# Kernel tuning notes

Hardware: AMD Instinct MI355X
Metric: run time of the kernel (lower is better)

Reference implementation:

```python
import jax, jax.numpy as jnp
import numpy as np

NUM_EVENT, EVENT_DIM = 6, 32
NUM_WORD, WORD_DIM = 100000, 128
NUM_SKU, SKU_DIM = 500000, 128
NUM_CAT, CAT_DIM = 10000, 64
NUM_PRICE, PRICE_DIM = 100, 32
NUM_URL, URL_DIM = 200000, 128
HIDDEN = 512
B, S, W = 256, 256, 12
PAD = 0


def _table(key, n, d):
    t = jax.random.normal(key, (n, d), dtype=jnp.float32) * 0.02
    return t.at[PAD].set(0.0)  # padding_idx row is zero


def setup_inputs() -> dict:
    key = jax.random.key(0)
    ks = jax.random.split(key, 20)
    inp = {
        "event_table": _table(ks[0], NUM_EVENT, EVENT_DIM),
        "word_table": _table(ks[1], NUM_WORD, WORD_DIM),
        "sku_table": _table(ks[2], NUM_SKU, SKU_DIM),
        "cat_table": _table(ks[3], NUM_CAT, CAT_DIM),
        "price_table": _table(ks[4], NUM_PRICE, PRICE_DIM),
        "url_table": _table(ks[5], NUM_URL, URL_DIM),
        # Linear weights, torch convention: y = x @ W.T + b
        "sku_w": jax.random.normal(ks[6], (HIDDEN, EVENT_DIM + SKU_DIM + CAT_DIM + PRICE_DIM + WORD_DIM), dtype=jnp.float32) * 0.02,
        "sku_b": jnp.zeros((HIDDEN,), dtype=jnp.float32),
        "url_w": jax.random.normal(ks[7], (HIDDEN, URL_DIM + EVENT_DIM), dtype=jnp.float32) * 0.02,
        "url_b": jnp.zeros((HIDDEN,), dtype=jnp.float32),
        "query_w": jax.random.normal(ks[8], (HIDDEN, EVENT_DIM + WORD_DIM), dtype=jnp.float32) * 0.02,
        "query_b": jnp.zeros((HIDDEN,), dtype=jnp.float32),
        "event_type": jax.random.randint(ks[9], (B, S), 0, NUM_EVENT, dtype=jnp.int32),
        "sku_id": jax.random.randint(ks[10], (B, S), 0, NUM_SKU, dtype=jnp.int32),
        "url_id": jax.random.randint(ks[11], (B, S), 0, NUM_URL, dtype=jnp.int32),
        "cat_id": jax.random.randint(ks[12], (B, S), 0, NUM_CAT, dtype=jnp.int32),
        "price_id": jax.random.randint(ks[13], (B, S), 0, NUM_PRICE, dtype=jnp.int32),
        "word_id": jax.random.randint(ks[14], (B, S, W), 0, NUM_WORD, dtype=jnp.int32),
    }
    return inp


def _linear_relu(x, w, b):
    return jax.nn.relu(jnp.einsum("bsi,hi->bsh", x, w) + b)


def reference(event_table, word_table, sku_table, cat_table, price_table, url_table,
              sku_w, sku_b, url_w, url_b, query_w, query_b,
              event_type, sku_id, url_id, cat_id, price_id, word_id):
    # padding mask: 1.0 where event_type == PAD_IDX
    src_padding_mask = (event_type == PAD).astype(jnp.float32)

    event_emb = event_table[event_type]                 # [B,S,E]
    word_emb = word_table[word_id].mean(axis=-2)        # [B,S,Wd] (WordEmbedding avg)

    # SKU branch (event types 1,2,3): concat(event, sku, cat, price, word)
    sku_in = jnp.concatenate([event_emb, sku_table[sku_id], cat_table[cat_id],
                              price_table[price_id], word_emb], axis=-1)
    sku_out = _linear_relu(sku_in, sku_w, sku_b)        # [B,S,H]

    # URL branch (event type 4): concat(url, event)  -- note order in UrlEmbedding
    url_in = jnp.concatenate([url_table[url_id], event_emb], axis=-1)
    url_out = _linear_relu(url_in, url_w, url_b)

    # Query branch (event type 5): concat(event, word)
    query_in = jnp.concatenate([event_emb, word_emb], axis=-1)
    query_out = _linear_relu(query_in, query_w, query_b)

    is_sku = ((event_type >= 1) & (event_type <= 3))[..., None]
    is_url = (event_type == 4)[..., None]
    is_query = (event_type == 5)[..., None]

    seq_emb = (jnp.where(is_sku, sku_out, 0.0)
               + jnp.where(is_url, url_out, 0.0)
               + jnp.where(is_query, query_out, 0.0))   # PAD positions stay zero
    return seq_emb, src_padding_mask
```

## Files before the change

### kernel.cpp

```cpp
#include <hip/hip_runtime.h>
#include <hip/hip_bf16.h>
#if !__has_builtin(__builtin_amdgcn_cvt_pk_fp8_f32) || !__has_builtin(__builtin_amdgcn_cvt_pk_f32_fp8)
#include <hip/hip_fp8.h>
#endif

#define CUR_OFF   0
#define SLOT_OFF  1024
#define POS_OFF   263168
#define WSKU_OFF  1049600
#define WURL_OFF  1246208
#define WQRY_OFF  1344512
#define WF8_OFF   2097152
#define XS_OFF    16777216
#define XU_OFF    50331648
#define XQ_OFF    68157440

#define NPOS      65536
#define OUT_MASK  33554432
#define F8_SCALE  64.0f
#define INV4096   (1.0f / 4096.0f)

typedef __attribute__((ext_vector_type(4))) float f32x4;
typedef __attribute__((ext_vector_type(2))) float f32x2;
typedef __attribute__((ext_vector_type(2))) unsigned int u32x2;

__device__ __forceinline__ float2 ld2(const float* p) {
    return *reinterpret_cast<const float2*>(p);
}

__device__ __forceinline__ unsigned int pk2_f8(float a, float b) {
#if __has_builtin(__builtin_amdgcn_cvt_pk_fp8_f32)
    return __builtin_amdgcn_cvt_pk_fp8_f32(a, b, 0u, false);
#else
    __hip_fp8_e4m3 fa(a), fb(b);
    return (unsigned int)fa.__x | ((unsigned int)fb.__x << 8);
#endif
}
__device__ __forceinline__ unsigned int pk4_f8(float a, float b, float c, float d) {
#if __has_builtin(__builtin_amdgcn_cvt_pk_fp8_f32)
    unsigned int v = 0;
    v = __builtin_amdgcn_cvt_pk_fp8_f32(a, b, v, false);
    v = __builtin_amdgcn_cvt_pk_fp8_f32(c, d, v, true);
    return v;
#else
    return pk2_f8(a, b) | (pk2_f8(c, d) << 16);
#endif
}
__device__ __forceinline__ float2 upk2_f8(unsigned int u) {
#if __has_builtin(__builtin_amdgcn_cvt_pk_f32_fp8)
    f32x2 r = __builtin_amdgcn_cvt_pk_f32_fp8(u, false);
    return make_float2(r.x, r.y);
#else
    __hip_fp8_e4m3 fa, fb;
    fa.__x = (unsigned char)(u & 0xff);
    fb.__x = (unsigned char)((u >> 8) & 0xff);
    return make_float2((float)fa, (float)fb);
#endif
}
__device__ __forceinline__ void st_f8x2(unsigned char* d, float a, float b) {
    *reinterpret_cast<unsigned short*>(d) = (unsigned short)(pk2_f8(a, b) & 0xffffu);
}

#define AS1(p) ((const __attribute__((address_space(1))) void*)(p))
#define AS3(p) ((__attribute__((address_space(3))) void*)(p))

__global__ __launch_bounds__(256) void prep_k(const float* __restrict__ sw,
                                              const float* __restrict__ uw,
                                              const float* __restrict__ qw,
                                              const float* __restrict__ word_t,
                                              char* ws) {
    const int b = blockIdx.x, t = threadIdx.x;
    if (b < 6250) {
        size_t i = ((size_t)b * 256 + t) * 8;
        f32x4 v0 = *reinterpret_cast<const f32x4*>(word_t + i);
        f32x4 v1 = *reinterpret_cast<const f32x4*>(word_t + i + 4);
        u32x2 pk;
        pk.x = pk4_f8(v0.x * F8_SCALE, v0.y * F8_SCALE, v0.z * F8_SCALE, v0.w * F8_SCALE);
        pk.y = pk4_f8(v1.x * F8_SCALE, v1.y * F8_SCALE, v1.z * F8_SCALE, v1.w * F8_SCALE);
        *reinterpret_cast<u32x2*>((unsigned char*)(ws + WF8_OFF) + i) = pk;
        return;
    }
    int tt = (b - 6250) * 256 + t;
    if (tt < 3) ((int*)(ws + CUR_OFF))[tt] = 0;
    if (tt < 196608) {
        ((unsigned char*)(ws + WSKU_OFF))[tt] =
            (unsigned char)(pk2_f8(sw[tt] * F8_SCALE, 0.f) & 0xffu);
    } else if (tt < 294912) {
        int i = tt - 196608; int n = i / 192, k = i % 192;
        ((unsigned char*)(ws + WURL_OFF))[i] = (k < 160)
            ? (unsigned char)(pk2_f8(uw[n * 160 + k] * F8_SCALE, 0.f) & 0xffu) : 0;
    } else {
        int i = tt - 294912; int n = i / 192, k = i % 192;
        ((unsigned char*)(ws + WQRY_OFF))[i] = (k < 160)
            ? (unsigned char)(pk2_f8(qw[n * 160 + k] * F8_SCALE, 0.f) & 0xffu) : 0;
    }
}

__global__ __launch_bounds__(256) void alloc_k(const int* __restrict__ et_a,
                                               float* __restrict__ out, char* ws) {
    __shared__ int s_wcnt[4][3];
    __shared__ int s_base[3];
    __shared__ int s_woff[4][3];
    const int t = threadIdx.x, lane = t & 63, wid = t >> 6;
    int p = blockIdx.x * 256 + t;
    int et = et_a[p];
    int br = (et >= 1 && et <= 3) ? 0 : (et == 4 ? 1 : (et == 5 ? 2 : -1));
    unsigned long long m0 = __ballot(br == 0);
    unsigned long long m1 = __ballot(br == 1);
    unsigned long long m2 = __ballot(br == 2);
    if (lane == 0) {
        s_wcnt[wid][0] = (int)__popcll(m0);
        s_wcnt[wid][1] = (int)__popcll(m1);
        s_wcnt[wid][2] = (int)__popcll(m2);
    }
    __syncthreads();
    if (t < 3) {
        int c0 = s_wcnt[0][t], c1 = s_wcnt[1][t], c2 = s_wcnt[2][t], c3 = s_wcnt[3][t];
        int tot = c0 + c1 + c2 + c3;
        s_base[t] = tot ? atomicAdd(&((int*)(ws + CUR_OFF))[t], tot) : 0;
        s_woff[0][t] = 0; s_woff[1][t] = c0; s_woff[2][t] = c0 + c1; s_woff[3][t] = c0 + c1 + c2;
    }
    __syncthreads();
    unsigned long long lt = (1ull << lane) - 1ull;
    int slot = -1;
    if (br == 0)      slot = s_base[0] + s_woff[wid][0] + (int)__popcll(m0 & lt);
    else if (br == 1) slot = s_base[1] + s_woff[wid][1] + (int)__popcll(m1 & lt);
    else if (br == 2) slot = s_base[2] + s_woff[wid][2] + (int)__popcll(m2 & lt);
    ((int*)(ws + SLOT_OFF))[p] = slot;
    if (slot >= 0) ((int*)(ws + POS_OFF))[br * NPOS + slot] = p;
    __builtin_nontemporal_store((et == 0) ? 1.0f : 0.0f, &out[OUT_MASK + p]);
}

__device__ __forceinline__ float2 wsum_f8(const unsigned char* __restrict__ wt8,
                                          const int* __restrict__ wids, int lane) {
    float sx = 0.f, sy = 0.f;
    #pragma unroll
    for (int k = 0; k < 12; ++k) {
        unsigned int u = *reinterpret_cast<const unsigned short*>(
            wt8 + (size_t)wids[k] * 128 + 2 * lane);
        float2 v = upk2_f8(u);
        sx += v.x; sy += v.y;
    }
    const float inv = 1.0f / 12.0f;
    return make_float2(sx * inv, sy * inv);
}

__global__ __launch_bounds__(256) void build_k(
    const float* __restrict__ ev_t,
    const float* __restrict__ sku_t,  const float* __restrict__ cat_t,
    const float* __restrict__ price_t,const float* __restrict__ url_t,
    const int* __restrict__ et_a,     const int* __restrict__ sku_id,
    const int* __restrict__ url_id,   const int* __restrict__ cat_id,
    const int* __restrict__ price_id, const int* __restrict__ word_id,
    float* __restrict__ out, char* ws)
{
    const int t = threadIdx.x, lane = t & 63, wid = t >> 6;
    const int p = blockIdx.x * 4 + wid;
    const int et = et_a[p];
    if (et == 0) {
        f32x4 z = {0.f, 0.f, 0.f, 0.f};
        float* orow = out + (size_t)p * 512;
        __builtin_nontemporal_store(z, reinterpret_cast<f32x4*>(&orow[lane * 8]));
        __builtin_nontemporal_store(z, reinterpret_cast<f32x4*>(&orow[lane * 8 + 4]));
        return;
    }
    const int slot = ((const int*)(ws + SLOT_OFF))[p];
    const unsigned char* wf8 = (const unsigned char*)(ws + WF8_OFF);
    const float* evr = ev_t + et * 32;
    if (et <= 3) {
        unsigned char* X = (unsigned char*)(ws + XS_OFF) + (size_t)slot * 384;
        if (lane < 16) { float2 e = ld2(evr + 2 * lane);
                         st_f8x2(X + 2 * lane, e.x * F8_SCALE, e.y * F8_SCALE); }
        const float* sr = sku_t + (size_t)sku_id[p] * 128;
        { float2 s = ld2(sr + 2 * lane);
          st_f8x2(X + 32 + 2 * lane, s.x * F8_SCALE, s.y * F8_SCALE); }
        if (lane < 32) { const float* cr = cat_t + (size_t)cat_id[p] * 64;
                         float2 c = ld2(cr + 2 * lane);
                         st_f8x2(X + 160 + 2 * lane, c.x * F8_SCALE, c.y * F8_SCALE); }
        if (lane < 16) { const float* pr = price_t + (size_t)price_id[p] * 32;
                         float2 v = ld2(pr + 2 * lane);
                         st_f8x2(X + 224 + 2 * lane, v.x * F8_SCALE, v.y * F8_SCALE); }
        float2 w = wsum_f8(wf8, word_id + (size_t)p * 12, lane);
        st_f8x2(X + 256 + 2 * lane, w.x, w.y);
    } else if (et == 4) {
        unsigned char* X = (unsigned char*)(ws + XU_OFF) + (size_t)slot * 192;
        const float* ur = url_t + (size_t)url_id[p] * 128;
        { float2 u = ld2(ur + 2 * lane);
          st_f8x2(X + 2 * lane, u.x * F8_SCALE, u.y * F8_SCALE); }
        if (lane < 16) { float2 e = ld2(evr + 2 * lane);
                         st_f8x2(X + 128 + 2 * lane, e.x * F8_SCALE, e.y * F8_SCALE); }
        if (lane >= 48) *reinterpret_cast<unsigned short*>(X + 160 + 2 * (lane - 48)) = 0;
    } else {
        unsigned char* X = (unsigned char*)(ws + XQ_OFF) + (size_t)slot * 192;
        if (lane < 16) { float2 e = ld2(evr + 2 * lane);
                         st_f8x2(X + 2 * lane, e.x * F8_SCALE, e.y * F8_SCALE); }
        float2 w = wsum_f8(wf8, word_id + (size_t)p * 12, lane);
        st_f8x2(X + 32 + 2 * lane, w.x, w.y);
        if (lane >= 48) *reinterpret_cast<unsigned short*>(X + 160 + 2 * (lane - 48)) = 0;
    }
}

__global__ __launch_bounds__(256, 2) void gemm_all_k(
    const char* __restrict__ ws_c, const float* __restrict__ sku_b,
    const float* __restrict__ url_b, const float* __restrict__ qry_b,
    float* __restrict__ out)
{
    const int z = blockIdx.z;
    const int count = ((const int*)(ws_c + CUR_OFF))[z];
    const int nmt = (count + 127) >> 7;
    const int nwg = nmt * 4;
    const int orig = blockIdx.x;
    if (orig >= nwg) return;
    const int q8 = nwg >> 3, r8 = nwg & 7;
    const int xcd = orig & 7, idx = orig >> 3;
    const int wg = (xcd < r8 ? xcd * (q8 + 1) : r8 * (q8 + 1) + (xcd - r8) * q8) + idx;
    const int mt = wg >> 2;
    const int row0 = mt * 128;
    const int nc0  = (wg & 3) * 128;

    const char* arena; const char* Wb; const float* bias; const int* posm;
    int astride, nkt;
    if (z == 0) { arena = ws_c + XS_OFF; Wb = ws_c + WSKU_OFF; bias = sku_b;
                  posm = (const int*)(ws_c + POS_OFF);          astride = 384; nkt = 3; }
    else if (z == 1) { arena = ws_c + XU_OFF; Wb = ws_c + WURL_OFF; bias = url_b;
                  posm = (const int*)(ws_c + POS_OFF) + NPOS;   astride = 192; nkt = 2; }
    else       { arena = ws_c + XQ_OFF; Wb = ws_c + WQRY_OFF; bias = qry_b;
                  posm = (const int*)(ws_c + POS_OFF) + 2*NPOS; astride = 192; nkt = 2; }

    __shared__ char lds[2][2][16384];

    const int t = threadIdx.x;
    const int lane = t & 63;
    const int wid  = t >> 6;
    const int wr = wid >> 1, wc = wid & 1;
    const int r = lane & 15, q = lane >> 4;

    auto stage = [&](int buf, int koff, bool full) {
        if (full) {
            #pragma unroll
            for (int i = 0; i < 4; ++i) {
                int row = i * 32 + (t >> 3);
                int sb  = (t & 7) ^ (row & 7);
                const char* ga = arena + (size_t)(row0 + row) * astride + koff + sb * 16;
                __builtin_amdgcn_global_load_lds(AS1(ga), AS3(&lds[buf][0][i * 4096 + t * 16]), 16, 0, 0);
                const char* gb = Wb + (size_t)(nc0 + row) * astride + koff + sb * 16;
                __builtin_amdgcn_global_load_lds(AS1(gb), AS3(&lds[buf][1][i * 4096 + t * 16]), 16, 0, 0);
            }
        } else {
            #pragma unroll
            for (int i = 0; i < 2; ++i) {
                int row = i * 64 + (t >> 2);
                int sb  = (t & 3) ^ (row & 3);
                const char* ga = arena + (size_t)(row0 + row) * astride + koff + sb * 16;
                __builtin_amdgcn_global_load_lds(AS1(ga), AS3(&lds[buf][0][i * 4096 + t * 16]), 16, 0, 0);
                const char* gb = Wb + (size_t)(nc0 + row) * astride + koff + sb * 16;
                __builtin_amdgcn_global_load_lds(AS1(gb), AS3(&lds[buf][1][i * 4096 + t * 16]), 16, 0, 0);
            }
        }
    };

    f32x4 acc[4][4];
    #pragma unroll
    for (int m = 0; m < 4; ++m)
        #pragma unroll
        for (int n = 0; n < 4; ++n)
            acc[m][n] = (f32x4){0.f, 0.f, 0.f, 0.f};

    stage(0, 0, true);
    __syncthreads();
    int cur = 0;
    for (int kt = 0; kt < nkt; ++kt) {
        const bool full = (z == 0) || (kt == 0);
        if (kt + 1 < nkt) stage(cur ^ 1, (kt + 1) * 128, (z == 0));
        if (full) {
            #pragma unroll
            for (int kk = 0; kk < 4; ++kk) {
                const int u  = kk * 2 + (q >> 1);
                const int wo = (q & 1) * 8;
                long af[4], bfr[4];
                #pragma unroll
                for (int m = 0; m < 4; ++m) {
                    int arow = wr * 64 + m * 16 + r;
                    af[m] = *reinterpret_cast<const long*>(
                        &lds[cur][0][arow * 128 + ((u ^ (arow & 7)) << 4) + wo]);
                }
                #pragma unroll
                for (int n = 0; n < 4; ++n) {
                    int brow = wc * 64 + n * 16 + r;
                    bfr[n] = *reinterpret_cast<const long*>(
                        &lds[cur][1][brow * 128 + ((u ^ (brow & 7)) << 4) + wo]);
                }
                #pragma unroll
                for (int m = 0; m < 4; ++m)
                    #pragma unroll
                    for (int n = 0; n < 4; ++n)
                        acc[m][n] = __builtin_amdgcn_mfma_f32_16x16x32_fp8_fp8(af[m], bfr[n], acc[m][n], 0, 0, 0);
            }
        } else {
            #pragma unroll
            for (int kk = 0; kk < 2; ++kk) {
                const int u  = kk * 2 + (q >> 1);
                const int wo = (q & 1) * 8;
                long af[4], bfr[4];
                #pragma unroll
                for (int m = 0; m < 4; ++m) {
                    int arow = wr * 64 + m * 16 + r;
                    af[m] = *reinterpret_cast<const long*>(
                        &lds[cur][0][arow * 64 + ((u ^ (arow & 3)) << 4) + wo]);
                }
                #pragma unroll
                for (int n = 0; n < 4; ++n) {
                    int brow = wc * 64 + n * 16 + r;
                    bfr[n] = *reinterpret_cast<const long*>(
                        &lds[cur][1][brow * 64 + ((u ^ (brow & 3)) << 4) + wo]);
                }
                #pragma unroll
                for (int m = 0; m < 4; ++m)
                    #pragma unroll
                    for (int n = 0; n < 4; ++n)
                        acc[m][n] = __builtin_amdgcn_mfma_f32_16x16x32_fp8_fp8(af[m], bfr[n], acc[m][n], 0, 0, 0);
            }
        }
        __syncthreads();
        cur ^= 1;
    }

    float bv[4];
    #pragma unroll
    for (int n = 0; n < 4; ++n) bv[n] = bias[nc0 + wc * 64 + n * 16 + r];
    #pragma unroll
    for (int m = 0; m < 4; ++m) {
        #pragma unroll
        for (int j = 0; j < 4; ++j) {
            int rl = wr * 64 + m * 16 + q * 4 + j;
            int gr = row0 + rl;
            if (gr < count) {
                int pos = posm[gr];
                float* orow = out + (size_t)pos * 512 + nc0 + wc * 64;
                #pragma unroll
                for (int n = 0; n < 4; ++n)
                    __builtin_nontemporal_store(
                        fmaxf(acc[m][n][j] * INV4096 + bv[n], 0.f), &orow[n * 16 + r]);
            }
        }
    }
}

extern "C" void kernel_launch(void* const* d_in, const int* in_sizes, int n_in,
                              void* d_out, int out_size, void* d_ws, size_t ws_size,
                              hipStream_t stream) {
    const float* ev_t    = (const float*)d_in[0];
    const float* word_t  = (const float*)d_in[1];
    const float* sku_t   = (const float*)d_in[2];
    const float* cat_t   = (const float*)d_in[3];
    const float* price_t = (const float*)d_in[4];
    const float* url_t   = (const float*)d_in[5];
    const float* sku_w   = (const float*)d_in[6];
    const float* sku_b   = (const float*)d_in[7];
    const float* url_w   = (const float*)d_in[8];
    const float* url_b   = (const float*)d_in[9];
    const float* query_w = (const float*)d_in[10];
    const float* query_b = (const float*)d_in[11];
    const int* event_type = (const int*)d_in[12];
    const int* sku_id     = (const int*)d_in[13];
    const int* url_id     = (const int*)d_in[14];
    const int* cat_id     = (const int*)d_in[15];
    const int* price_id   = (const int*)d_in[16];
    const int* word_id    = (const int*)d_in[17];

    char*  ws  = (char*)d_ws;
    float* out = (float*)d_out;

    prep_k<<<7786, 256, 0, stream>>>(sku_w, url_w, query_w, word_t, ws);
    alloc_k<<<256, 256, 0, stream>>>(event_type, out, ws);
    build_k<<<16384, 256, 0, stream>>>(ev_t, sku_t, cat_t, price_t, url_t,
                                       event_type, sku_id, url_id, cat_id, price_id,
                                       word_id, out, ws);
    dim3 gg(2048, 1, 3);
    gemm_all_k<<<gg, 256, 0, stream>>>(ws, sku_b, url_b, query_b, out);
}
```

Baseline: 86.76 us.

## Unroll GEMM K-loop with explicit vmcnt waits and raw barriers

Replaces the generic double-buffered K loop with fully unrolled per-branch schedules that issue two stages up front and use partial s_waitcnt vmcnt counts plus raw s_barrier instead of __syncthreads. This lets the second tile's async global-to-LDS loads stay in flight while the first tile is computed, removing full memory drains at each step. It relies on hand-counted outstanding load numbers and sched_barrier fences, so any miscount or compiler-inserted memory op could cause races.

After: 86.21 us (median of 2 runs). Within noise of the previous version (-0.6%).

```diff
diff --git a/kernel.cpp b/kernel.cpp
--- a/kernel.cpp
+++ b/kernel.cpp
@@ -63,6 +63,13 @@
 
 #define AS1(p) ((const __attribute__((address_space(1))) void*)(p))
 #define AS3(p) ((__attribute__((address_space(3))) void*)(p))
+
+#define WAITV0() asm volatile("s_waitcnt vmcnt(0)" ::: "memory")
+#define WAITV4() asm volatile("s_waitcnt vmcnt(4)" ::: "memory")
+#define WAITV8() asm volatile("s_waitcnt vmcnt(8)" ::: "memory")
+#define WAITL()  asm volatile("s_waitcnt lgkmcnt(0)" ::: "memory")
+#define BARR()   __builtin_amdgcn_s_barrier()
+#define FENCE()  __builtin_amdgcn_sched_barrier(0)
 
 __global__ __launch_bounds__(256) void prep_k(const float* __restrict__ sw,
                                               const float* __restrict__ uw,
@@ -219,13 +226,13 @@
     const int nc0  = (wg & 3) * 128;
 
     const char* arena; const char* Wb; const float* bias; const int* posm;
-    int astride, nkt;
+    int astride;
     if (z == 0) { arena = ws_c + XS_OFF; Wb = ws_c + WSKU_OFF; bias = sku_b;
-                  posm = (const int*)(ws_c + POS_OFF);          astride = 384; nkt = 3; }
+                  posm = (const int*)(ws_c + POS_OFF);          astride = 384; }
     else if (z == 1) { arena = ws_c + XU_OFF; Wb = ws_c + WURL_OFF; bias = url_b;
-                  posm = (const int*)(ws_c + POS_OFF) + NPOS;   astride = 192; nkt = 2; }
+                  posm = (const int*)(ws_c + POS_OFF) + NPOS;   astride = 192; }
     else       { arena = ws_c + XQ_OFF; Wb = ws_c + WQRY_OFF; bias = qry_b;
-                  posm = (const int*)(ws_c + POS_OFF) + 2*NPOS; astride = 192; nkt = 2; }
+                  posm = (const int*)(ws_c + POS_OFF) + 2*NPOS; astride = 192; }
 
     __shared__ char lds[2][2][16384];
 
@@ -235,27 +242,26 @@
     const int wr = wid >> 1, wc = wid & 1;
     const int r = lane & 15, q = lane >> 4;
 
-    auto stage = [&](int buf, int koff, bool full) {
-        if (full) {
-            #pragma unroll
-            for (int i = 0; i < 4; ++i) {
-                int row = i * 32 + (t >> 3);
-                int sb  = (t & 7) ^ (row & 7);
-                const char* ga = arena + (size_t)(row0 + row) * astride + koff + sb * 16;
-                __builtin_amdgcn_global_load_lds(AS1(ga), AS3(&lds[buf][0][i * 4096 + t * 16]), 16, 0, 0);
-                const char* gb = Wb + (size_t)(nc0 + row) * astride + koff + sb * 16;
-                __builtin_amdgcn_global_load_lds(AS1(gb), AS3(&lds[buf][1][i * 4096 + t * 16]), 16, 0, 0);
-            }
-        } else {
-            #pragma unroll
-            for (int i = 0; i < 2; ++i) {
-                int row = i * 64 + (t >> 2);
-                int sb  = (t & 3) ^ (row & 3);
-                const char* ga = arena + (size_t)(row0 + row) * astride + koff + sb * 16;
-                __builtin_amdgcn_global_load_lds(AS1(ga), AS3(&lds[buf][0][i * 4096 + t * 16]), 16, 0, 0);
-                const char* gb = Wb + (size_t)(nc0 + row) * astride + koff + sb * 16;
-                __builtin_amdgcn_global_load_lds(AS1(gb), AS3(&lds[buf][1][i * 4096 + t * 16]), 16, 0, 0);
-            }
+    auto stage_full = [&](int buf, int koff) {
+        #pragma unroll
+        for (int i = 0; i < 4; ++i) {
+            int row = i * 32 + (t >> 3);
+            int sb  = (t & 7) ^ (row & 7);
+            const char* ga = arena + (size_t)(row0 + row) * astride + koff + sb * 16;
+            __builtin_amdgcn_global_load_lds(AS1(ga), AS3(&lds[buf][0][i * 4096 + t * 16]), 16, 0, 0);
+            const char* gb = Wb + (size_t)(nc0 + row) * astride + koff + sb * 16;
+            __builtin_amdgcn_global_load_lds(AS1(gb), AS3(&lds[buf][1][i * 4096 + t * 16]), 16, 0, 0);
+        }
+    };
+    auto stage_half = [&](int buf, int koff) {
+        #pragma unroll
+        for (int i = 0; i < 2; ++i) {
+            int row = i * 64 + (t >> 2);
+            int sb  = (t & 3) ^ (row & 3);
+            const char* ga = arena + (size_t)(row0 + row) * astride + koff + sb * 16;
+            __builtin_amdgcn_global_load_lds(AS1(ga), AS3(&lds[buf][0][i * 4096 + t * 16]), 16, 0, 0);
+            const char* gb = Wb + (size_t)(nc0 + row) * astride + koff + sb * 16;
+            __builtin_amdgcn_global_load_lds(AS1(gb), AS3(&lds[buf][1][i * 4096 + t * 16]), 16, 0, 0);
         }
     };
 
@@ -266,63 +272,75 @@
         for (int n = 0; n < 4; ++n)
             acc[m][n] = (f32x4){0.f, 0.f, 0.f, 0.f};
 
-    stage(0, 0, true);
-    __syncthreads();
-    int cur = 0;
-    for (int kt = 0; kt < nkt; ++kt) {
-        const bool full = (z == 0) || (kt == 0);
-        if (kt + 1 < nkt) stage(cur ^ 1, (kt + 1) * 128, (z == 0));
-        if (full) {
-            #pragma unroll
-            for (int kk = 0; kk < 4; ++kk) {
-                const int u  = kk * 2 + (q >> 1);
-                const int wo = (q & 1) * 8;
-                long af[4], bfr[4];
+    auto comp_full = [&](int buf) {
+        #pragma unroll
+        for (int kk = 0; kk < 4; ++kk) {
+            const int u  = kk * 2 + (q >> 1);
+            const int wo = (q & 1) * 8;
+            long af[4], bfr[4];
+            #pragma unroll
+            for (int m = 0; m < 4; ++m) {
+                int arow = wr * 64 + m * 16 + r;
+                af[m] = *reinterpret_cast<const long*>(
+                    &lds[buf][0][arow * 128 + ((u ^ (arow & 7)) << 4) + wo]);
+            }
+            #pragma unroll
+            for (int n = 0; n < 4; ++n) {
+                int brow = wc * 64 + n * 16 + r;
+                bfr[n] = *reinterpret_cast<const long*>(
+                    &lds[buf][1][brow * 128 + ((u ^ (brow & 7)) << 4) + wo]);
+            }
+            #pragma unroll
+            for (int m = 0; m < 4; ++m)
                 #pragma unroll
-                for (int m = 0; m < 4; ++m) {
-                    int arow = wr * 64 + m * 16 + r;
-                    af[m] = *reinterpret_cast<const long*>(
-                        &lds[cur][0][arow * 128 + ((u ^ (arow & 7)) << 4) + wo]);
-                }
+                for (int n = 0; n < 4; ++n)
+                    acc[m][n] = __builtin_amdgcn_mfma_f32_16x16x32_fp8_fp8(af[m], bfr[n], acc[m][n], 0, 0, 0);
+        }
+    };
+    auto comp_half = [&](int buf) {
+        #pragma unroll
+        for (int kk = 0; kk < 2; ++kk) {
+            const int u  = kk * 2 + (q >> 1);
+            const int wo = (q & 1) * 8;
+            long af[4], bfr[4];
+            #pragma unroll
+            for (int m = 0; m < 4; ++m) {
+                int arow = wr * 64 + m * 16 + r;
+                af[m] = *reinterpret_cast<const long*>(
+                    &lds[buf][0][arow * 64 + ((u ^ (arow & 3)) << 4) + wo]);
+            }
+            #pragma unroll
+            for (int n = 0; n < 4; ++n) {
+                int brow = wc * 64 + n * 16 + r;
+                bfr[n] = *reinterpret_cast<const long*>(
+                    &lds[buf][1][brow * 64 + ((u ^ (brow & 3)) << 4) + wo]);
+            }
+            #pragma unroll
+            for (int m = 0; m < 4; ++m)
                 #pragma unroll
-                for (int n = 0; n < 4; ++n) {
-                    int brow = wc * 64 + n * 16 + r;
-                    bfr[n] = *reinterpret_cast<const long*>(
-                        &lds[cur][1][brow * 128 + ((u ^ (brow & 7)) << 4) + wo]);
-                }
-                #pragma unroll
-                for (int m = 0; m < 4; ++m)
-                    #pragma unroll
-                    for (int n = 0; n < 4; ++n)
-                        acc[m][n] = __builtin_amdgcn_mfma_f32_16x16x32_fp8_fp8(af[m], bfr[n], acc[m][n], 0, 0, 0);
-            }
-        } else {
-            #pragma unroll
-            for (int kk = 0; kk < 2; ++kk) {
-                const int u  = kk * 2 + (q >> 1);
-                const int wo = (q & 1) * 8;
-                long af[4], bfr[4];
-                #pragma unroll
-                for (int m = 0; m < 4; ++m) {
-                    int arow = wr * 64 + m * 16 + r;
-                    af[m] = *reinterpret_cast<const long*>(
-                        &lds[cur][0][arow * 64 + ((u ^ (arow & 3)) << 4) + wo]);
-                }
-                #pragma unroll
-                for (int n = 0; n < 4; ++n) {
-                    int brow = wc * 64 + n * 16 + r;
-                    bfr[n] = *reinterpret_cast<const long*>(
-                        &lds[cur][1][brow * 64 + ((u ^ (brow & 3)) << 4) + wo]);
-                }
-                #pragma unroll
-                for (int m = 0; m < 4; ++m)
-                    #pragma unroll
-                    for (int n = 0; n < 4; ++n)
-                        acc[m][n] = __builtin_amdgcn_mfma_f32_16x16x32_fp8_fp8(af[m], bfr[n], acc[m][n], 0, 0, 0);
-            }
-        }
-        __syncthreads();
-        cur ^= 1;
+                for (int n = 0; n < 4; ++n)
+                    acc[m][n] = __builtin_amdgcn_mfma_f32_16x16x32_fp8_fp8(af[m], bfr[n], acc[m][n], 0, 0, 0);
+        }
+    };
+
+    if (z == 0) {
+        stage_full(0, 0);
+        stage_full(1, 128);
+        WAITV8(); BARR(); FENCE();
+        comp_full(0);
+        WAITL(); BARR(); FENCE();
+        stage_full(0, 256);
+        WAITV8(); BARR(); FENCE();
+        comp_full(1);
+        WAITV0(); BARR(); FENCE();
+        comp_full(0);
+    } else {
+        stage_full(0, 0);
+        stage_half(1, 128);
+        WAITV4(); BARR(); FENCE();
+        comp_full(0);
+        WAITV0(); BARR(); FENCE();
+        comp_half(1);
     }
 
     float bv[4];
```

## Fuse embedding gather into GEMM, keeping A tile resident across all N chunks

Applied to the files above, without the earlier changes.

The separate build kernel that gathered embeddings into fp8 staging arenas in global memory is removed. The GEMM kernel now gathers each 128-row A tile directly into LDS once and loops over all four 128-column N chunks, streaming only the weight tiles with double buffering. Zeroing of padding rows moves into the allocation kernel. This removes the global round trip for the activation matrix and one kernel launch, but the gather is now serialized inside the GEMM blocks, and the grid shrinks fourfold with more LDS per block.

New measurement: 137.0 us. +57.9%, slower.

```diff
diff --git a/kernel.cpp b/kernel.cpp
--- a/kernel.cpp
+++ b/kernel.cpp
@@ -11,9 +11,6 @@
 #define WURL_OFF  1246208
 #define WQRY_OFF  1344512
 #define WF8_OFF   2097152
-#define XS_OFF    16777216
-#define XU_OFF    50331648
-#define XQ_OFF    68157440
 
 #define NPOS      65536
 #define OUT_MASK  33554432
@@ -56,9 +53,6 @@
     fb.__x = (unsigned char)((u >> 8) & 0xff);
     return make_float2((float)fa, (float)fb);
 #endif
-}
-__device__ __forceinline__ void st_f8x2(unsigned char* d, float a, float b) {
-    *reinterpret_cast<unsigned short*>(d) = (unsigned short)(pk2_f8(a, b) & 0xffffu);
 }
 
 #define AS1(p) ((const __attribute__((address_space(1))) void*)(p))
@@ -101,9 +95,12 @@
     __shared__ int s_wcnt[4][3];
     __shared__ int s_base[3];
     __shared__ int s_woff[4][3];
+    __shared__ int s_et[256];
     const int t = threadIdx.x, lane = t & 63, wid = t >> 6;
-    int p = blockIdx.x * 256 + t;
+    const int p0 = blockIdx.x * 256;
+    int p = p0 + t;
     int et = et_a[p];
+    s_et[t] = et;
     int br = (et >= 1 && et <= 3) ? 0 : (et == 4 ? 1 : (et == 5 ? 2 : -1));
     unsigned long long m0 = __ballot(br == 0);
     unsigned long long m1 = __ballot(br == 1);
@@ -129,6 +126,14 @@
     ((int*)(ws + SLOT_OFF))[p] = slot;
     if (slot >= 0) ((int*)(ws + POS_OFF))[br * NPOS + slot] = p;
     __builtin_nontemporal_store((et == 0) ? 1.0f : 0.0f, &out[OUT_MASK + p]);
+    for (int i = wid; i < 256; i += 4) {
+        if (s_et[i] == 0) {
+            float* orow = out + (size_t)(p0 + i) * 512;
+            f32x4 z = {0.f, 0.f, 0.f, 0.f};
+            __builtin_nontemporal_store(z, reinterpret_cast<f32x4*>(&orow[lane * 8]));
+            __builtin_nontemporal_store(z, reinterpret_cast<f32x4*>(&orow[lane * 8 + 4]));
+        }
+    }
 }
 
 __device__ __forceinline__ float2 wsum_f8(const unsigned char* __restrict__ wt8,
@@ -145,203 +150,227 @@
     return make_float2(sx * inv, sy * inv);
 }
 
-__global__ __launch_bounds__(256) void build_k(
-    const float* __restrict__ ev_t,
-    const float* __restrict__ sku_t,  const float* __restrict__ cat_t,
-    const float* __restrict__ price_t,const float* __restrict__ url_t,
+__global__ __launch_bounds__(256, 2) void ggemm_k(
+    const char* __restrict__ ws_c,
+    const float* __restrict__ ev_t,   const float* __restrict__ sku_t,
+    const float* __restrict__ cat_t,  const float* __restrict__ price_t,
+    const float* __restrict__ url_t,
     const int* __restrict__ et_a,     const int* __restrict__ sku_id,
     const int* __restrict__ url_id,   const int* __restrict__ cat_id,
     const int* __restrict__ price_id, const int* __restrict__ word_id,
-    float* __restrict__ out, char* ws)
-{
-    const int t = threadIdx.x, lane = t & 63, wid = t >> 6;
-    const int p = blockIdx.x * 4 + wid;
-    const int et = et_a[p];
-    if (et == 0) {
-        f32x4 z = {0.f, 0.f, 0.f, 0.f};
-        float* orow = out + (size_t)p * 512;
-        __builtin_nontemporal_store(z, reinterpret_cast<f32x4*>(&orow[lane * 8]));
-        __builtin_nontemporal_store(z, reinterpret_cast<f32x4*>(&orow[lane * 8 + 4]));
-        return;
-    }
-    const int slot = ((const int*)(ws + SLOT_OFF))[p];
-    const unsigned char* wf8 = (const unsigned char*)(ws + WF8_OFF);
-    const float* evr = ev_t + et * 32;
-    if (et <= 3) {
-        unsigned char* X = (unsigned char*)(ws + XS_OFF) + (size_t)slot * 384;
-        if (lane < 16) { float2 e = ld2(evr + 2 * lane);
-                         st_f8x2(X + 2 * lane, e.x * F8_SCALE, e.y * F8_SCALE); }
-        const float* sr = sku_t + (size_t)sku_id[p] * 128;
-        { float2 s = ld2(sr + 2 * lane);
-          st_f8x2(X + 32 + 2 * lane, s.x * F8_SCALE, s.y * F8_SCALE); }
-        if (lane < 32) { const float* cr = cat_t + (size_t)cat_id[p] * 64;
-                         float2 c = ld2(cr + 2 * lane);
-                         st_f8x2(X + 160 + 2 * lane, c.x * F8_SCALE, c.y * F8_SCALE); }
-        if (lane < 16) { const float* pr = price_t + (size_t)price_id[p] * 32;
-                         float2 v = ld2(pr + 2 * lane);
-                         st_f8x2(X + 224 + 2 * lane, v.x * F8_SCALE, v.y * F8_SCALE); }
-        float2 w = wsum_f8(wf8, word_id + (size_t)p * 12, lane);
-        st_f8x2(X + 256 + 2 * lane, w.x, w.y);
-    } else if (et == 4) {
-        unsigned char* X = (unsigned char*)(ws + XU_OFF) + (size_t)slot * 192;
-        const float* ur = url_t + (size_t)url_id[p] * 128;
-        { float2 u = ld2(ur + 2 * lane);
-          st_f8x2(X + 2 * lane, u.x * F8_SCALE, u.y * F8_SCALE); }
-        if (lane < 16) { float2 e = ld2(evr + 2 * lane);
-                         st_f8x2(X + 128 + 2 * lane, e.x * F8_SCALE, e.y * F8_SCALE); }
-        if (lane >= 48) *reinterpret_cast<unsigned short*>(X + 160 + 2 * (lane - 48)) = 0;
-    } else {
-        unsigned char* X = (unsigned char*)(ws + XQ_OFF) + (size_t)slot * 192;
-        if (lane < 16) { float2 e = ld2(evr + 2 * lane);
-                         st_f8x2(X + 2 * lane, e.x * F8_SCALE, e.y * F8_SCALE); }
-        float2 w = wsum_f8(wf8, word_id + (size_t)p * 12, lane);
-        st_f8x2(X + 32 + 2 * lane, w.x, w.y);
-        if (lane >= 48) *reinterpret_cast<unsigned short*>(X + 160 + 2 * (lane - 48)) = 0;
-    }
-}
-
-__global__ __launch_bounds__(256, 2) void gemm_all_k(
-    const char* __restrict__ ws_c, const float* __restrict__ sku_b,
-    const float* __restrict__ url_b, const float* __restrict__ qry_b,
-    float* __restrict__ out)
+    const float* __restrict__ sku_b,  const float* __restrict__ url_b,
+    const float* __restrict__ qry_b,  float* __restrict__ out)
 {
     const int z = blockIdx.z;
     const int count = ((const int*)(ws_c + CUR_OFF))[z];
     const int nmt = (count + 127) >> 7;
-    const int nwg = nmt * 4;
     const int orig = blockIdx.x;
-    if (orig >= nwg) return;
-    const int q8 = nwg >> 3, r8 = nwg & 7;
+    if (orig >= nmt) return;
+    const int q8 = nmt >> 3, r8 = nmt & 7;
     const int xcd = orig & 7, idx = orig >> 3;
-    const int wg = (xcd < r8 ? xcd * (q8 + 1) : r8 * (q8 + 1) + (xcd - r8) * q8) + idx;
-    const int mt = wg >> 2;
+    const int mt = (xcd < r8 ? xcd * (q8 + 1) : r8 * (q8 + 1) + (xcd - r8) * q8) + idx;
     const int row0 = mt * 128;
-    const int nc0  = (wg & 3) * 128;
-
-    const char* arena; const char* Wb; const float* bias; const int* posm;
-    int astride, nkt;
-    if (z == 0) { arena = ws_c + XS_OFF; Wb = ws_c + WSKU_OFF; bias = sku_b;
-                  posm = (const int*)(ws_c + POS_OFF);          astride = 384; nkt = 3; }
-    else if (z == 1) { arena = ws_c + XU_OFF; Wb = ws_c + WURL_OFF; bias = url_b;
-                  posm = (const int*)(ws_c + POS_OFF) + NPOS;   astride = 192; nkt = 2; }
-    else       { arena = ws_c + XQ_OFF; Wb = ws_c + WQRY_OFF; bias = qry_b;
-                  posm = (const int*)(ws_c + POS_OFF) + 2*NPOS; astride = 192; nkt = 2; }
-
-    __shared__ char lds[2][2][16384];
-
-    const int t = threadIdx.x;
-    const int lane = t & 63;
-    const int wid  = t >> 6;
+
+    const int* posm = (const int*)(ws_c + POS_OFF) + z * NPOS;
+    const unsigned char* wf8 = (const unsigned char*)(ws_c + WF8_OFF);
+    const char* Wb; const float* bias; int wstride;
+    if (z == 0)      { Wb = ws_c + WSKU_OFF; bias = sku_b; wstride = 384; }
+    else if (z == 1) { Wb = ws_c + WURL_OFF; bias = url_b; wstride = 192; }
+    else             { Wb = ws_c + WQRY_OFF; bias = qry_b; wstride = 192; }
+
+    __shared__ char ldsA[49152];
+    __shared__ char ldsB[2][16384];
+
+    const int t = threadIdx.x, lane = t & 63, wid = t >> 6;
     const int wr = wid >> 1, wc = wid & 1;
     const int r = lane & 15, q = lane >> 4;
 
-    auto stage = [&](int buf, int koff, bool full) {
-        if (full) {
-            #pragma unroll
-            for (int i = 0; i < 4; ++i) {
-                int row = i * 32 + (t >> 3);
-                int sb  = (t & 7) ^ (row & 7);
-                const char* ga = arena + (size_t)(row0 + row) * astride + koff + sb * 16;
-                __builtin_amdgcn_global_load_lds(AS1(ga), AS3(&lds[buf][0][i * 4096 + t * 16]), 16, 0, 0);
-                const char* gb = Wb + (size_t)(nc0 + row) * astride + koff + sb * 16;
-                __builtin_amdgcn_global_load_lds(AS1(gb), AS3(&lds[buf][1][i * 4096 + t * 16]), 16, 0, 0);
-            }
+    auto stA384 = [&](int row, int off, unsigned int pk) {
+        int kt = off >> 7, o = off & 127, u = o >> 4;
+        int addr = kt * 16384 + row * 128 + (((u ^ (row & 7)) << 4) | (o & 15));
+        *reinterpret_cast<unsigned short*>(ldsA + addr) = (unsigned short)(pk & 0xffffu);
+    };
+    auto stA192 = [&](int row, int off, unsigned int pk) {
+        int addr;
+        if (off < 128) { int u = off >> 4;
+            addr = row * 128 + (((u ^ (row & 7)) << 4) | (off & 15)); }
+        else { int o = off - 128; int u = o >> 4;
+            addr = 16384 + row * 64 + (((u ^ (row & 3)) << 4) | (o & 15)); }
+        *reinterpret_cast<unsigned short*>(ldsA + addr) = (unsigned short)(pk & 0xffffu);
+    };
+
+    auto stageB_full = [&](int buf, int nc, int koff) {
+        #pragma unroll
+        for (int i = 0; i < 4; ++i) {
+            int row = i * 32 + (t >> 3);
+            int sb  = (t & 7) ^ (row & 7);
+            const char* gb = Wb + (size_t)(nc * 128 + row) * wstride + koff + sb * 16;
+            __builtin_amdgcn_global_load_lds(AS1(gb), AS3(&ldsB[buf][i * 4096 + t * 16]), 16, 0, 0);
+        }
+    };
+    auto stageB_half = [&](int buf, int nc, int koff) {
+        #pragma unroll
+        for (int i = 0; i < 2; ++i) {
+            int row = i * 64 + (t >> 2);
+            int sb  = (t & 3) ^ (row & 3);
+            const char* gb = Wb + (size_t)(nc * 128 + row) * wstride + koff + sb * 16;
+            __builtin_amdgcn_global_load_lds(AS1(gb), AS3(&ldsB[buf][i * 4096 + t * 16]), 16, 0, 0);
+        }
+    };
+
+    stageB_full(0, 0, 0);
+    if (z == 0) stageB_full(1, 0, 128); else stageB_half(1, 0, 128);
+
+    for (int i = 0; i < 32; ++i) {
+        int row = (wid << 5) + i;
+        int gr  = row0 + row;
+        if (gr >= count) break;
+        int p = posm[gr];
+        if (z == 0) {
+            int et = et_a[p];
+            const float* evr = ev_t + et * 32;
+            if (lane < 16) { float2 e = ld2(evr + 2 * lane);
+                stA384(row, 2 * lane, pk2_f8(e.x * F8_SCALE, e.y * F8_SCALE)); }
+            { float2 s = ld2(sku_t + (size_t)sku_id[p] * 128 + 2 * lane);
+                stA384(row, 32 + 2 * lane, pk2_f8(s.x * F8_SCALE, s.y * F8_SCALE)); }
+            if (lane < 32) { float2 c = ld2(cat_t + (size_t)cat_id[p] * 64 + 2 * lane);
+                stA384(row, 160 + 2 * lane, pk2_f8(c.x * F8_SCALE, c.y * F8_SCALE)); }
+            if (lane < 16) { float2 v = ld2(price_t + (size_t)price_id[p] * 32 + 2 * lane);
+                stA384(row, 224 + 2 * lane, pk2_f8(v.x * F8_SCALE, v.y * F8_SCALE)); }
+            float2 w = wsum_f8(wf8, word_id + (size_t)p * 12, lane);
+            stA384(row, 256 + 2 * lane, pk2_f8(w.x, w.y));
+        } else if (z == 1) {
+            const float* evr = ev_t + 4 * 32;
+            { float2 u = ld2(url_t + (size_t)url_id[p] * 128 + 2 * lane);
+                stA192(row, 2 * lane, pk2_f8(u.x * F8_SCALE, u.y * F8_SCALE)); }
+            if (lane < 16) { float2 e = ld2(evr + 2 * lane);
+                stA192(row, 128 + 2 * lane, pk2_f8(e.x * F8_SCALE, e.y * F8_SCALE)); }
+            if (lane >= 48) stA192(row, 160 + 2 * (lane - 48), 0u);
         } else {
-            #pragma unroll
-            for (int i = 0; i < 2; ++i) {
-                int row = i * 64 + (t >> 2);
-                int sb  = (t & 3) ^ (row & 3);
-                const char* ga = arena + (size_t)(row0 + row) * astride + koff + sb * 16;
-                __builtin_amdgcn_global_load_lds(AS1(ga), AS3(&lds[buf][0][i * 4096 + t * 16]), 16, 0, 0);
-                const char* gb = Wb + (size_t)(nc0 + row) * astride + koff + sb * 16;
-                __builtin_amdgcn_global_load_lds(AS1(gb), AS3(&lds[buf][1][i * 4096 + t * 16]), 16, 0, 0);
-            }
-        }
-    };
-
-    f32x4 acc[4][4];
+            const float* evr = ev_t + 5 * 32;
+            if (lane < 16) { float2 e = ld2(evr + 2 * lane);
+                stA192(row, 2 * lane, pk2_f8(e.x * F8_SCALE, e.y * F8_SCALE)); }
+            float2 w = wsum_f8(wf8, word_id + (size_t)p * 12, lane);
+            stA192(row, 32 + 2 * lane, pk2_f8(w.x, w.y));
+            if (lane >= 48) stA192(row, 160 + 2 * (lane - 48), 0u);
+        }
+    }
+    __syncthreads();
+
+    int posr[16];
     #pragma unroll
     for (int m = 0; m < 4; ++m)
         #pragma unroll
-        for (int n = 0; n < 4; ++n)
-            acc[m][n] = (f32x4){0.f, 0.f, 0.f, 0.f};
-
-    stage(0, 0, true);
-    __syncthreads();
-    int cur = 0;
-    for (int kt = 0; kt < nkt; ++kt) {
-        const bool full = (z == 0) || (kt == 0);
-        if (kt + 1 < nkt) stage(cur ^ 1, (kt + 1) * 128, (z == 0));
-        if (full) {
-            #pragma unroll
-            for (int kk = 0; kk < 4; ++kk) {
-                const int u  = kk * 2 + (q >> 1);
-                const int wo = (q & 1) * 8;
-                long af[4], bfr[4];
+        for (int j = 0; j < 4; ++j) {
+            int gr = row0 + wr * 64 + m * 16 + q * 4 + j;
+            posr[m * 4 + j] = (gr < count) ? posm[gr] : -1;
+        }
+
+    f32x4 acc[4][4];
+    auto compA_full = [&](int ktA, int buf) {
+        #pragma unroll
+        for (int kk = 0; kk < 4; ++kk) {
+            const int u  = kk * 2 + (q >> 1);
+            const int wo = (q & 1) * 8;
+            long af[4], bf[4];
+            #pragma unroll
+            for (int m = 0; m < 4; ++m) {
+                int arow = wr * 64 + m * 16 + r;
+                af[m] = *reinterpret_cast<const long*>(
+                    &ldsA[ktA * 16384 + arow * 128 + ((u ^ (arow & 7)) << 4) + wo]);
+            }
+            #pragma unroll
+            for (int n = 0; n < 4; ++n) {
+                int brow = wc * 64 + n * 16 + r;
+                bf[n] = *reinterpret_cast<const long*>(
+                    &ldsB[buf][brow * 128 + ((u ^ (brow & 7)) << 4) + wo]);
+            }
+            #pragma unroll
+            for (int m = 0; m < 4; ++m)
                 #pragma unroll
-                for (int m = 0; m < 4; ++m) {
-                    int arow = wr * 64 + m * 16 + r;
-                    af[m] = *reinterpret_cast<const long*>(
-                        &lds[cur][0][arow * 128 + ((u ^ (arow & 7)) << 4) + wo]);
-                }
+                for (int n = 0; n < 4; ++n)
+                    acc[m][n] = __builtin_amdgcn_mfma_f32_16x16x32_fp8_fp8(af[m], bf[n], acc[m][n], 0, 0, 0);
+        }
+    };
+    auto compA_half = [&](int buf) {
+        #pragma unroll
+        for (int kk = 0; kk < 2; ++kk) {
+            const int u  = kk * 2 + (q >> 1);
+            const int wo = (q & 1) * 8;
+            long af[4], bf[4];
+            #pragma unroll
+            for (int m = 0; m < 4; ++m) {
+                int arow = wr * 64 + m * 16 + r;
+                af[m] = *reinterpret_cast<const long*>(
+                    &ldsA[16384 + arow * 64 + ((u ^ (arow & 3)) << 4) + wo]);
+            }
+            #pragma unroll
+            for (int n = 0; n < 4; ++n) {
+                int brow = wc * 64 + n * 16 + r;
+                bf[n] = *reinterpret_cast<const long*>(
+                    &ldsB[buf][brow * 64 + ((u ^ (brow & 3)) << 4) + wo]);
+            }
+            #pragma unroll
+            for (int m = 0; m < 4; ++m)
                 #pragma unroll
-                for (int n = 0; n < 4; ++n) {
-                    int brow = wc * 64 + n * 16 + r;
-                    bfr[n] = *reinterpret_cast<const long*>(
-                        &lds[cur][1][brow * 128 + ((u ^ (brow & 7)) << 4) + wo]);
-                }
-                #pragma unroll
-                for (int m = 0; m < 4; ++m)
+                for (int n = 0; n < 4; ++n)
+                    acc[m][n] = __builtin_amdgcn_mfma_f32_16x16x32_fp8_fp8(af[m], bf[n], acc[m][n], 0, 0, 0);
+        }
+    };
+    auto epilogue = [&](int nc) {
+        float bv[4];
+        #pragma unroll
+        for (int n = 0; n < 4; ++n) bv[n] = bias[nc * 128 + wc * 64 + n * 16 + r];
+        #pragma unroll
+        for (int m = 0; m < 4; ++m)
+            #pragma unroll
+            for (int j = 0; j < 4; ++j) {
+                int pos = posr[m * 4 + j];
+                if (pos >= 0) {
+                    float* orow = out + (size_t)pos * 512 + nc * 128 + wc * 64;
                     #pragma unroll
                     for (int n = 0; n < 4; ++n)
-                        acc[m][n] = __builtin_amdgcn_mfma_f32_16x16x32_fp8_fp8(af[m], bfr[n], acc[m][n], 0, 0, 0);
-            }
-        } else {
-            #pragma unroll
-            for (int kk = 0; kk < 2; ++kk) {
-                const int u  = kk * 2 + (q >> 1);
-                const int wo = (q & 1) * 8;
-                long af[4], bfr[4];
-                #pragma unroll
-                for (int m = 0; m < 4; ++m) {
-                    int arow = wr * 64 + m * 16 + r;
-                    af[m] = *reinterpret_cast<const long*>(
-                        &lds[cur][0][arow * 64 + ((u ^ (arow & 3)) << 4) + wo]);
+                        __builtin_nontemporal_store(
+                            fmaxf(acc[m][n][j] * INV4096 + bv[n], 0.f), &orow[n * 16 + r]);
                 }
-                #pragma unroll
-                for (int n = 0; n < 4; ++n) {
-                    int brow = wc * 64 + n * 16 + r;
-                    bfr[n] = *reinterpret_cast<const long*>(
-                        &lds[cur][1][brow * 64 + ((u ^ (brow & 3)) << 4) + wo]);
-                }
-                #pragma unroll
-                for (int m = 0; m < 4; ++m)
-                    #pragma unroll
-                    for (int n = 0; n < 4; ++n)
-                        acc[m][n] = __builtin_amdgcn_mfma_f32_16x16x32_fp8_fp8(af[m], bfr[n], acc[m][n], 0, 0, 0);
-            }
-        }
-        __syncthreads();
-        cur ^= 1;
-    }
-
-    float bv[4];
-    #pragma unroll
-    for (int n = 0; n < 4; ++n) bv[n] = bias[nc0 + wc * 64 + n * 16 + r];
-    #pragma unroll
-    for (int m = 0; m < 4; ++m) {
-        #pragma unroll
-        for (int j = 0; j < 4; ++j) {
-            int rl = wr * 64 + m * 16 + q * 4 + j;
-            int gr = row0 + rl;
-            if (gr < count) {
-                int pos = posm[gr];
-                float* orow = out + (size_t)pos * 512 + nc0 + wc * 64;
+            }
+    };
+
+    if (z == 0) {
+        for (int nc = 0; nc < 4; ++nc) {
+            #pragma unroll
+            for (int m = 0; m < 4; ++m)
                 #pragma unroll
                 for (int n = 0; n < 4; ++n)
-                    __builtin_nontemporal_store(
-                        fmaxf(acc[m][n][j] * INV4096 + bv[n], 0.f), &orow[n * 16 + r]);
-            }
+                    acc[m][n] = (f32x4){0.f, 0.f, 0.f, 0.f};
+            #pragma unroll
+            for (int kt = 0; kt < 3; ++kt) {
+                int j = nc * 3 + kt, jn = j + 1;
+                if (jn < 12) stageB_full(jn & 1, jn / 3, (jn % 3) * 128);
+                compA_full(kt, j & 1);
+                __syncthreads();
+            }
+            epilogue(nc);
+        }
+    } else {
+        for (int nc = 0; nc < 4; ++nc) {
+            #pragma unroll
+            for (int m = 0; m < 4; ++m)
+                #pragma unroll
+                for (int n = 0; n < 4; ++n)
+                    acc[m][n] = (f32x4){0.f, 0.f, 0.f, 0.f};
+            #pragma unroll
+            for (int kt = 0; kt < 2; ++kt) {
+                int j = nc * 2 + kt, jn = j + 1;
+                if (jn < 8) {
+                    if ((jn & 1) == 0) stageB_full(jn & 1, jn / 2, 0);
+                    else               stageB_half(jn & 1, jn / 2, 128);
+                }
+                if (kt == 0) compA_full(0, j & 1);
+                else         compA_half(j & 1);
+                __syncthreads();
+            }
+            epilogue(nc);
         }
     }
 }
@@ -373,9 +402,8 @@
 
     prep_k<<<7786, 256, 0, stream>>>(sku_w, url_w, query_w, word_t, ws);
     alloc_k<<<256, 256, 0, stream>>>(event_type, out, ws);
-    build_k<<<16384, 256, 0, stream>>>(ev_t, sku_t, cat_t, price_t, url_t,
-                                       event_type, sku_id, url_id, cat_id, price_id,
-                                       word_id, out, ws);
-    dim3 gg(2048, 1, 3);
-    gemm_all_k<<<gg, 256, 0, stream>>>(ws, sku_b, url_b, query_b, out);
-}
+    dim3 gg(512, 1, 3);
+    ggemm_k<<<gg, 256, 0, stream>>>(ws, ev_t, sku_t, cat_t, price_t, url_t,
+                                    event_type, sku_id, url_id, cat_id, price_id,
+                                    word_id, sku_b, url_b, query_b, out);
+}
```
